# Kernel optimization log

Measured on AMD Instinct MI355X. Metric: run time of the kernel, lower is better.

## Reference

```python
import jax, jax.numpy as jnp
import numpy as np

DECAY = 0.99
EPS = 1e-05
COMMIT = 0.25


def setup_inputs() -> dict:
    key = jax.random.key(0)
    k1, k2 = jax.random.split(key)
    dim, n_embed = 256, 8192
    z = jax.random.normal(k1, (32, 32, 32, dim), dtype=jnp.float32)
    embed = jax.random.normal(k2, (dim, n_embed), dtype=jnp.float32)
    cluster_size = jnp.zeros((n_embed,), dtype=jnp.float32)
    embed_avg = embed  # torch init: embed_avg = embed.clone()
    return {"z": z, "embed": embed, "cluster_size": cluster_size, "embed_avg": embed_avg}


def reference(z, embed, cluster_size, embed_avg):
    dim, n_embed = embed.shape
    flatten = z.reshape(-1, dim)                       # [N, D]
    # squared L2 distance to each code: ||f||^2 - 2 f.E + ||E||^2
    dist = ((flatten ** 2).sum(1, keepdims=True)
            - 2.0 * flatten @ embed
            + (embed ** 2).sum(0, keepdims=True))      # [N, K]
    ind = jnp.argmin(dist, axis=1)                     # [N]
    quantize = jnp.take(embed.T, ind, axis=0).reshape(z.shape)
    embed_ind = ind.reshape(z.shape[:-1])

    # EMA codebook update (training mode), via segment_sum instead of a dense one-hot
    counts = jax.ops.segment_sum(jnp.ones_like(ind, dtype=flatten.dtype), ind,
                                 num_segments=n_embed)          # [K]
    embed_sum = jax.ops.segment_sum(flatten, ind,
                                    num_segments=n_embed).T     # [D, K]
    cluster_size_new = cluster_size * DECAY + (1.0 - DECAY) * counts
    embed_avg_new = embed_avg * DECAY + (1.0 - DECAY) * embed_sum
    n = cluster_size_new.sum()
    cs = (cluster_size_new + EPS) / (n + n_embed * EPS) * n
    embed_new = embed_avg_new / cs[None, :]

    diff = COMMIT * jnp.mean((jax.lax.stop_gradient(quantize) - z) ** 2)
    quantize_st = z + jax.lax.stop_gradient(quantize - z)  # straight-through
    return quantize_st, diff, embed_ind, embed_new
```

## Files before the change

### kernel.cpp

```cpp
#include <hip/hip_runtime.h>
#include <hip/hip_bf16.h>

#define D 256
#define K 8192
#define NTOT 32768
#define BM 128
#define BN2 128
#define BD 32
#define CSPLIT 4
#define CT_PER (K / CSPLIT / BN2)

typedef __bf16 bf16x8 __attribute__((ext_vector_type(8)));
typedef float f32x4 __attribute__((ext_vector_type(4)));

__device__ __forceinline__ void gl_lds16(const void* g, void* l) {
    __builtin_amdgcn_global_load_lds(
        (__attribute__((address_space(1))) void*)(g),
        (__attribute__((address_space(3))) void*)(l), 16, 0, 0);
}

__device__ __forceinline__ unsigned int enc_f32(float f) {
    unsigned int u = __float_as_uint(f);
    return (u & 0x80000000u) ? ~u : (u | 0x80000000u);
}

__device__ __forceinline__ unsigned short f2bfu(float x) {
    __hip_bfloat16 h = __float2bfloat16(x);
    return __builtin_bit_cast(unsigned short, h);
}
__device__ __forceinline__ float bfu2f(unsigned short u) {
    return __bfloat162float(__builtin_bit_cast(__hip_bfloat16, u));
}

__global__ __launch_bounds__(256)
void conv_F(const float* __restrict__ z, unsigned short* __restrict__ Fhi,
            unsigned short* __restrict__ Flo) {
    int i4 = blockIdx.x * 256 + threadIdx.x;
    float4 v = ((const float4*)z)[i4];
    ushort4 h, l;
    h.x = f2bfu(v.x); l.x = f2bfu(v.x - bfu2f(h.x));
    h.y = f2bfu(v.y); l.y = f2bfu(v.y - bfu2f(h.y));
    h.z = f2bfu(v.z); l.z = f2bfu(v.z - bfu2f(h.z));
    h.w = f2bfu(v.w); l.w = f2bfu(v.w - bfu2f(h.w));
    ((ushort4*)Fhi)[i4] = h;
    ((ushort4*)Flo)[i4] = l;
}

__global__ __launch_bounds__(256)
void conv_E(const float* __restrict__ E, unsigned short* __restrict__ EhiT,
            unsigned short* __restrict__ EloT, float* __restrict__ ET) {
    __shared__ float tile[64][65];
    int tid = threadIdx.x;
    int k0 = blockIdx.x * 64, d0 = blockIdx.y * 64;
#pragma unroll
    for (int it = 0; it < 16; ++it) {
        int idx = it * 256 + tid;
        int dr = idx >> 6, kc = idx & 63;
        tile[kc][dr] = E[(d0 + dr) * K + k0 + kc];
    }
    __syncthreads();
#pragma unroll
    for (int it = 0; it < 16; ++it) {
        int idx = it * 256 + tid;
        int kr = idx >> 6, dc = idx & 63;
        float v = tile[kr][dc];
        unsigned short h = f2bfu(v);
        int o = (k0 + kr) * D + d0 + dc;
        EhiT[o] = h;
        EloT[o] = f2bfu(v - bfu2f(h));
        ET[o] = v;
    }
}

__global__ __launch_bounds__(256)
void enorm_kernel(const float* __restrict__ E, float* __restrict__ enorm) {
    int k = blockIdx.x * 256 + threadIdx.x;
    float s = 0.f;
    for (int d = 0; d < D; ++d) {
        float v = E[d * K + k];
        s += v * v;
    }
    enorm[k] = s;
}

__global__ __launch_bounds__(256)
void mfma_dist_argmin(const unsigned short* __restrict__ Fhi,
                      const unsigned short* __restrict__ Flo,
                      const unsigned short* __restrict__ EhiT,
                      const unsigned short* __restrict__ EloT,
                      const float* __restrict__ enorm,
                      unsigned long long* __restrict__ bestpack) {
    __shared__ unsigned short Ah[BM * BD], Al[BM * BD], Bh[BN2 * BD], Bl[BN2 * BD];

    const int tid = threadIdx.x;
    const int wave = tid >> 6;
    const int lane = tid & 63;
    const int qd = lane >> 4;
    const int ln = lane & 15;
    const int wm = (wave >> 1) * 64;
    const int wn = (wave & 1) * 64;
    const int n0 = blockIdx.x * BM;
    const int c0 = blockIdx.y * (K / CSPLIT);
    const int r_ = tid >> 2, s_ = tid & 3;

    float bestv[16];
    int besti[16];
#pragma unroll
    for (int i = 0; i < 16; ++i) { bestv[i] = 3.402823466e38f; besti[i] = 0; }

    for (int ct = 0; ct < CT_PER; ++ct) {
        const int cb = c0 + ct * BN2;
        f32x4 acc[4][4];
#pragma unroll
        for (int mi = 0; mi < 4; ++mi)
#pragma unroll
            for (int ni = 0; ni < 4; ++ni) acc[mi][ni] = (f32x4){0.f, 0.f, 0.f, 0.f};

        for (int d0 = 0; d0 < D; d0 += BD) {
#pragma unroll
            for (int it = 0; it < 2; ++it) {
                const int row = it * 64 + r_;
                const int goffA = (n0 + row) * D + d0 + s_ * 8;
                const int goffB = (cb + row) * D + d0 + s_ * 8;
                const int loff = it * 2048 + wave * 512;
                gl_lds16(Fhi + goffA, &Ah[loff]);
                gl_lds16(Flo + goffA, &Al[loff]);
                gl_lds16(EhiT + goffB, &Bh[loff]);
                gl_lds16(EloT + goffB, &Bl[loff]);
            }
            __syncthreads();

            bf16x8 ah[4], al[4], bh[4], bl[4];
#pragma unroll
            for (int mi = 0; mi < 4; ++mi) {
                int off = (wm + mi * 16 + ln) * BD + qd * 8;
                ah[mi] = *(const bf16x8*)&Ah[off];
                al[mi] = *(const bf16x8*)&Al[off];
            }
#pragma unroll
            for (int ni = 0; ni < 4; ++ni) {
                int off = (wn + ni * 16 + ln) * BD + qd * 8;
                bh[ni] = *(const bf16x8*)&Bh[off];
                bl[ni] = *(const bf16x8*)&Bl[off];
            }
#pragma unroll
            for (int mi = 0; mi < 4; ++mi)
#pragma unroll
                for (int ni = 0; ni < 4; ++ni)
                    acc[mi][ni] = __builtin_amdgcn_mfma_f32_16x16x32_bf16(
                        ah[mi], bh[ni], acc[mi][ni], 0, 0, 0);
#pragma unroll
            for (int mi = 0; mi < 4; ++mi)
#pragma unroll
                for (int ni = 0; ni < 4; ++ni)
                    acc[mi][ni] = __builtin_amdgcn_mfma_f32_16x16x32_bf16(
                        ah[mi], bl[ni], acc[mi][ni], 0, 0, 0);
#pragma unroll
            for (int mi = 0; mi < 4; ++mi)
#pragma unroll
                for (int ni = 0; ni < 4; ++ni)
                    acc[mi][ni] = __builtin_amdgcn_mfma_f32_16x16x32_bf16(
                        al[mi], bh[ni], acc[mi][ni], 0, 0, 0);
            __syncthreads();
        }

#pragma unroll
        for (int ni = 0; ni < 4; ++ni) {
            int k = cb + wn + ni * 16 + ln;
            float en = enorm[k];
#pragma unroll
            for (int mi = 0; mi < 4; ++mi) {
                f32x4 a = acc[mi][ni];
#pragma unroll
                for (int r = 0; r < 4; ++r) {
                    float dist = en - 2.0f * a[r];
                    int bi = mi * 4 + r;
                    if (dist < bestv[bi]) { bestv[bi] = dist; besti[bi] = k; }
                }
            }
        }
    }

#pragma unroll
    for (int mi = 0; mi < 4; ++mi) {
#pragma unroll
        for (int r = 0; r < 4; ++r) {
            int bi = mi * 4 + r;
            float v = bestv[bi];
            int ix = besti[bi];
#pragma unroll
            for (int off = 1; off < 16; off <<= 1) {
                float v2 = __shfl_xor(v, off);
                int i2 = __shfl_xor(ix, off);
                if (v2 < v || (v2 == v && i2 < ix)) { v = v2; ix = i2; }
            }
            if (ln == 0) {
                int m = n0 + wm + mi * 16 + qd * 4 + r;
                unsigned long long pack =
                    ((unsigned long long)enc_f32(v) << 32) | (unsigned int)ix;
                atomicMin(&bestpack[m], pack);
            }
        }
    }
}

#define ROWS_PER_BLOCK 64
__global__ __launch_bounds__(256)
void assign_apply(const float* __restrict__ z,
                  const float* __restrict__ ET,
                  const unsigned long long* __restrict__ bestpack,
                  float* __restrict__ out_q, float* __restrict__ out_ind,
                  float* __restrict__ out_diff,
                  float* __restrict__ counts, float* __restrict__ esumT) {
    const int tx = threadIdx.x;
    const int rbase = blockIdx.x * ROWS_PER_BLOCK;
    float part = 0.f;
    for (int r = 0; r < ROWS_PER_BLOCK; ++r) {
        int n = rbase + r;
        unsigned long long p = bestpack[n];
        int idx = (int)(p & 0xFFFFFFFFull);
        float f = z[n * D + tx];
        float q = ET[idx * D + tx];
        out_q[n * D + tx] = q;
        float dd = q - f;
        part += dd * dd;
        atomicAdd(&esumT[idx * D + tx], f);
        if (tx == 0) {
            atomicAdd(&counts[idx], 1.0f);
            out_ind[n] = (float)idx;
        }
    }
#pragma unroll
    for (int off = 32; off; off >>= 1) part += __shfl_down(part, off);
    __shared__ float wsum[4];
    if ((tx & 63) == 0) wsum[tx >> 6] = part;
    __syncthreads();
    if (tx == 0) {
        float t = wsum[0] + wsum[1] + wsum[2] + wsum[3];
        atomicAdd(out_diff, t * (0.25f / 8388608.0f));
    }
}

__global__ __launch_bounds__(1024)
void csn_sum(const float* __restrict__ cs_in, const float* __restrict__ counts,
             float* __restrict__ csn, float* __restrict__ nsum) {
    const float decay = 0.99f;
    const float omd = 0.01f;
    int tx = threadIdx.x;
    float p = 0.f;
    for (int k = tx; k < K; k += 1024) {
        float v = decay * cs_in[k] + omd * counts[k];
        csn[k] = v;
        p += v;
    }
#pragma unroll
    for (int off = 32; off; off >>= 1) p += __shfl_down(p, off);
    __shared__ float red[16];
    if ((tx & 63) == 0) red[tx >> 6] = p;
    __syncthreads();
    if (tx == 0) {
        float t = 0.f;
        for (int i = 0; i < 16; ++i) t += red[i];
        nsum[0] = t;
    }
}

__global__ __launch_bounds__(256)
void finalize(const float* __restrict__ eavg, const float* __restrict__ esumT,
              const float* __restrict__ csn, const float* __restrict__ nsum,
              float* __restrict__ out_enew) {
    const float decay = 0.99f;
    const float omd = 0.01f;
    const float keps = (float)(8192 * 1e-5);
    int idx = blockIdx.x * 256 + threadIdx.x;
    float nv = nsum[0];
    int k = idx & (K - 1);
    int d = idx >> 13;
    float avg_new = decay * eavg[idx] + omd * esumT[k * D + d];
    float cs = (csn[k] + 1e-5f) / (nv + keps) * nv;
    out_enew[idx] = avg_new / cs;
}

extern "C" void kernel_launch(void* const* d_in, const int* in_sizes, int n_in,
                              void* d_out, int out_size, void* d_ws, size_t ws_size,
                              hipStream_t stream) {
    const float* z = (const float*)d_in[0];
    const float* embed = (const float*)d_in[1];
    const float* cs_in = (const float*)d_in[2];
    const float* eavg = (const float*)d_in[3];

    float* out = (float*)d_out;
    float* out_q = out;
    float* out_diff = out + 8388608;
    float* out_ind = out + 8388609;
    float* out_enew = out + 8421377;

    char* ws = (char*)d_ws;
    unsigned long long* bestpack = (unsigned long long*)ws;
    float* enorm = (float*)(ws + 262144);
    float* counts = (float*)(ws + 294912);
    float* csn = (float*)(ws + 327680);
    float* nsum = (float*)(ws + 360448);
    float* esumT = (float*)(ws + 360704);
    unsigned short* Fhi = (unsigned short*)(ws + 8749312);
    unsigned short* Flo = (unsigned short*)(ws + 25526528);
    unsigned short* EhiT = (unsigned short*)(ws + 42303744);
    unsigned short* EloT = (unsigned short*)(ws + 46498048);
    float* ET = (float*)(ws + 50692352);

    hipMemsetAsync(bestpack, 0xFF, NTOT * 8, stream);
    hipMemsetAsync(counts, 0, K * 4, stream);
    hipMemsetAsync(esumT, 0, K * D * 4, stream);
    hipMemsetAsync(out_diff, 0, 4, stream);

    conv_F<<<NTOT * D / 4 / 256, 256, 0, stream>>>(z, Fhi, Flo);
    conv_E<<<dim3(K / 64, D / 64), 256, 0, stream>>>(embed, EhiT, EloT, ET);
    enorm_kernel<<<K / 256, 256, 0, stream>>>(embed, enorm);
    mfma_dist_argmin<<<dim3(NTOT / BM, CSPLIT), 256, 0, stream>>>(Fhi, Flo, EhiT, EloT,
                                                                  enorm, bestpack);
    assign_apply<<<NTOT / ROWS_PER_BLOCK, 256, 0, stream>>>(z, ET, bestpack, out_q,
                                                            out_ind, out_diff, counts, esumT);
    csn_sum<<<1, 1024, 0, stream>>>(cs_in, counts, csn, nsum);
    finalize<<<(D * K) / 256, 256, 0, stream>>>(eavg, esumT, csn, nsum, out_enew);
}
```

Measured before the change: 612.8 us.

## Load MFMA operands directly from global into registers with double buffering

Drops the shared-memory staging and barriers in the distance/argmin GEMM. Each wave now loads its bf16 hi/lo operand fragments straight from global memory into registers, prefetching the next K-slice into a second register buffer while the current one feeds the MFMAs. Launch bounds now request two blocks per CU. Each wave pulls its own copy of the shared tiles, so data reuse across waves now depends on cache instead of LDS, and the doubled register buffers raise register pressure.

```diff
diff --git a/kernel.cpp b/kernel.cpp
--- a/kernel.cpp
+++ b/kernel.cpp
@@ -6,18 +6,11 @@
 #define NTOT 32768
 #define BM 128
 #define BN2 128
-#define BD 32
 #define CSPLIT 4
 #define CT_PER (K / CSPLIT / BN2)
 
 typedef __bf16 bf16x8 __attribute__((ext_vector_type(8)));
 typedef float f32x4 __attribute__((ext_vector_type(4)));
-
-__device__ __forceinline__ void gl_lds16(const void* g, void* l) {
-    __builtin_amdgcn_global_load_lds(
-        (__attribute__((address_space(1))) void*)(g),
-        (__attribute__((address_space(3))) void*)(l), 16, 0, 0);
-}
 
 __device__ __forceinline__ unsigned int enc_f32(float f) {
     unsigned int u = __float_as_uint(f);
@@ -83,15 +76,13 @@
     enorm[k] = s;
 }
 
-__global__ __launch_bounds__(256)
+__global__ __launch_bounds__(256, 2)
 void mfma_dist_argmin(const unsigned short* __restrict__ Fhi,
                       const unsigned short* __restrict__ Flo,
                       const unsigned short* __restrict__ EhiT,
                       const unsigned short* __restrict__ EloT,
                       const float* __restrict__ enorm,
                       unsigned long long* __restrict__ bestpack) {
-    __shared__ unsigned short Ah[BM * BD], Al[BM * BD], Bh[BN2 * BD], Bl[BN2 * BD];
-
     const int tid = threadIdx.x;
     const int wave = tid >> 6;
     const int lane = tid & 63;
@@ -101,79 +92,84 @@
     const int wn = (wave & 1) * 64;
     const int n0 = blockIdx.x * BM;
     const int c0 = blockIdx.y * (K / CSPLIT);
-    const int r_ = tid >> 2, s_ = tid & 3;
+
+    int aoff[4], boff[4];
+#pragma unroll
+    for (int mi = 0; mi < 4; ++mi) aoff[mi] = (n0 + wm + mi * 16 + ln) * D + qd * 8;
+#pragma unroll
+    for (int ni = 0; ni < 4; ++ni) boff[ni] = (wn + ni * 16 + ln) * D + qd * 8;
 
     float bestv[16];
     int besti[16];
 #pragma unroll
     for (int i = 0; i < 16; ++i) { bestv[i] = 3.402823466e38f; besti[i] = 0; }
 
+    bf16x8 ah[2][4], al[2][4], bh[2][4], bl[2][4];
+
+    auto load_stage = [&](int buf, int ct, int d0) {
+        const int ub = (c0 + ct * BN2) * D + d0;
+#pragma unroll
+        for (int mi = 0; mi < 4; ++mi) {
+            ah[buf][mi] = *(const bf16x8*)(Fhi + aoff[mi] + d0);
+            al[buf][mi] = *(const bf16x8*)(Flo + aoff[mi] + d0);
+        }
+#pragma unroll
+        for (int ni = 0; ni < 4; ++ni) {
+            bh[buf][ni] = *(const bf16x8*)(EhiT + boff[ni] + ub);
+            bl[buf][ni] = *(const bf16x8*)(EloT + boff[ni] + ub);
+        }
+    };
+
+    load_stage(0, 0, 0);
+
     for (int ct = 0; ct < CT_PER; ++ct) {
         const int cb = c0 + ct * BN2;
+        float en[4];
+#pragma unroll
+        for (int ni = 0; ni < 4; ++ni) en[ni] = enorm[cb + wn + ni * 16 + ln];
+
         f32x4 acc[4][4];
 #pragma unroll
         for (int mi = 0; mi < 4; ++mi)
 #pragma unroll
             for (int ni = 0; ni < 4; ++ni) acc[mi][ni] = (f32x4){0.f, 0.f, 0.f, 0.f};
 
-        for (int d0 = 0; d0 < D; d0 += BD) {
-#pragma unroll
-            for (int it = 0; it < 2; ++it) {
-                const int row = it * 64 + r_;
-                const int goffA = (n0 + row) * D + d0 + s_ * 8;
-                const int goffB = (cb + row) * D + d0 + s_ * 8;
-                const int loff = it * 2048 + wave * 512;
-                gl_lds16(Fhi + goffA, &Ah[loff]);
-                gl_lds16(Flo + goffA, &Al[loff]);
-                gl_lds16(EhiT + goffB, &Bh[loff]);
-                gl_lds16(EloT + goffB, &Bl[loff]);
-            }
-            __syncthreads();
-
-            bf16x8 ah[4], al[4], bh[4], bl[4];
-#pragma unroll
-            for (int mi = 0; mi < 4; ++mi) {
-                int off = (wm + mi * 16 + ln) * BD + qd * 8;
-                ah[mi] = *(const bf16x8*)&Ah[off];
-                al[mi] = *(const bf16x8*)&Al[off];
-            }
-#pragma unroll
-            for (int ni = 0; ni < 4; ++ni) {
-                int off = (wn + ni * 16 + ln) * BD + qd * 8;
-                bh[ni] = *(const bf16x8*)&Bh[off];
-                bl[ni] = *(const bf16x8*)&Bl[off];
-            }
+#pragma unroll
+        for (int dd = 0; dd < 8; ++dd) {
+            const int b = dd & 1;
+            int nct = ct, ndd = dd + 1;
+            if (ndd == 8) { ndd = 0; nct = ct + 1; }
+            if (nct < CT_PER) load_stage(b ^ 1, nct, ndd * 32);
+
 #pragma unroll
             for (int mi = 0; mi < 4; ++mi)
 #pragma unroll
                 for (int ni = 0; ni < 4; ++ni)
                     acc[mi][ni] = __builtin_amdgcn_mfma_f32_16x16x32_bf16(
-                        ah[mi], bh[ni], acc[mi][ni], 0, 0, 0);
+                        ah[b][mi], bh[b][ni], acc[mi][ni], 0, 0, 0);
 #pragma unroll
             for (int mi = 0; mi < 4; ++mi)
 #pragma unroll
                 for (int ni = 0; ni < 4; ++ni)
                     acc[mi][ni] = __builtin_amdgcn_mfma_f32_16x16x32_bf16(
-                        ah[mi], bl[ni], acc[mi][ni], 0, 0, 0);
+                        ah[b][mi], bl[b][ni], acc[mi][ni], 0, 0, 0);
 #pragma unroll
             for (int mi = 0; mi < 4; ++mi)
 #pragma unroll
                 for (int ni = 0; ni < 4; ++ni)
                     acc[mi][ni] = __builtin_amdgcn_mfma_f32_16x16x32_bf16(
-                        al[mi], bh[ni], acc[mi][ni], 0, 0, 0);
-            __syncthreads();
+                        al[b][mi], bh[b][ni], acc[mi][ni], 0, 0, 0);
         }
 
 #pragma unroll
         for (int ni = 0; ni < 4; ++ni) {
             int k = cb + wn + ni * 16 + ln;
-            float en = enorm[k];
 #pragma unroll
             for (int mi = 0; mi < 4; ++mi) {
                 f32x4 a = acc[mi][ni];
 #pragma unroll
                 for (int r = 0; r < 4; ++r) {
-                    float dist = en - 2.0f * a[r];
+                    float dist = en[ni] - 2.0f * a[r];
                     int bi = mi * 4 + r;
                     if (dist < bestv[bi]) { bestv[bi] = dist; besti[bi] = k; }
                 }
```

Result: slower. 1.279 ms (+108.7%).

## Swizzle LDS tiles in distance GEMM and read enorm from transposed codebook

Applied to the files above, without the earlier changes.

The distance/argmin kernel now XOR-swizzles the 16-byte chunk position within each LDS row, both when loading and when reading fragments, to cut LDS bank conflicts. It also moves the barrier to the top of the d-loop and preloads the enorm values before the argmin epilogue. enorm_kernel now reads rows of the transposed fp32 codebook with float4 loads instead of strided columns. conv_E gains a partial-sum reduction that only atomically adds zero, so that work is dead and adds some atomics.

```diff
diff --git a/kernel.cpp b/kernel.cpp
--- a/kernel.cpp
+++ b/kernel.cpp
@@ -48,7 +48,8 @@
 
 __global__ __launch_bounds__(256)
 void conv_E(const float* __restrict__ E, unsigned short* __restrict__ EhiT,
-            unsigned short* __restrict__ EloT, float* __restrict__ ET) {
+            unsigned short* __restrict__ EloT, float* __restrict__ ET,
+            float* __restrict__ enorm) {
     __shared__ float tile[64][65];
     int tid = threadIdx.x;
     int k0 = blockIdx.x * 64, d0 = blockIdx.y * 64;
@@ -59,6 +60,7 @@
         tile[kc][dr] = E[(d0 + dr) * K + k0 + kc];
     }
     __syncthreads();
+    float psum[4];
 #pragma unroll
     for (int it = 0; it < 16; ++it) {
         int idx = it * 256 + tid;
@@ -69,16 +71,29 @@
         EhiT[o] = h;
         EloT[o] = f2bfu(v - bfu2f(h));
         ET[o] = v;
-    }
-}
-
-__global__ __launch_bounds__(256)
-void enorm_kernel(const float* __restrict__ E, float* __restrict__ enorm) {
+        psum[it & 3] = (it < 4 ? 0.f : psum[it & 3]) + v * v;
+    }
+#pragma unroll
+    for (int g = 0; g < 4; ++g) {
+        float p = psum[g];
+#pragma unroll
+        for (int off = 32; off; off >>= 1) p += __shfl_down(p, off);
+        if ((tid & 63) == 0) {
+            int kr = g * 4 + (tid >> 6);
+            atomicAdd(&enorm[k0 + kr * 4 + 0], 0.f);
+        }
+    }
+}
+
+__global__ __launch_bounds__(256)
+void enorm_kernel(const float* __restrict__ ET, float* __restrict__ enorm) {
     int k = blockIdx.x * 256 + threadIdx.x;
+    const float4* row = (const float4*)(ET + k * D);
     float s = 0.f;
-    for (int d = 0; d < D; ++d) {
-        float v = E[d * K + k];
-        s += v * v;
+#pragma unroll
+    for (int d = 0; d < D / 4; ++d) {
+        float4 v = row[d];
+        s += v.x * v.x + v.y * v.y + v.z * v.z + v.w * v.w;
     }
     enorm[k] = s;
 }
@@ -101,7 +116,9 @@
     const int wn = (wave & 1) * 64;
     const int n0 = blockIdx.x * BM;
     const int c0 = blockIdx.y * (K / CSPLIT);
-    const int r_ = tid >> 2, s_ = tid & 3;
+    const int r_ = tid >> 2;
+    const int s_sw = (tid & 3) ^ ((tid >> 3) & 3);
+    const int csw = (qd ^ ((ln >> 1) & 3)) * 8;
 
     float bestv[16];
     int besti[16];
@@ -117,29 +134,29 @@
             for (int ni = 0; ni < 4; ++ni) acc[mi][ni] = (f32x4){0.f, 0.f, 0.f, 0.f};
 
         for (int d0 = 0; d0 < D; d0 += BD) {
+            __syncthreads();
 #pragma unroll
             for (int it = 0; it < 2; ++it) {
-                const int row = it * 64 + r_;
-                const int goffA = (n0 + row) * D + d0 + s_ * 8;
-                const int goffB = (cb + row) * D + d0 + s_ * 8;
-                const int loff = it * 2048 + wave * 512;
-                gl_lds16(Fhi + goffA, &Ah[loff]);
-                gl_lds16(Flo + goffA, &Al[loff]);
-                gl_lds16(EhiT + goffB, &Bh[loff]);
-                gl_lds16(EloT + goffB, &Bl[loff]);
+                const int ga = (n0 + it * 64 + r_) * D + d0 + s_sw * 8;
+                const int gb = (cb + it * 64 + r_) * D + d0 + s_sw * 8;
+                const int lo = it * 2048 + wave * 512;
+                gl_lds16(Fhi + ga, &Ah[lo]);
+                gl_lds16(Flo + ga, &Al[lo]);
+                gl_lds16(EhiT + gb, &Bh[lo]);
+                gl_lds16(EloT + gb, &Bl[lo]);
             }
             __syncthreads();
 
             bf16x8 ah[4], al[4], bh[4], bl[4];
 #pragma unroll
             for (int mi = 0; mi < 4; ++mi) {
-                int off = (wm + mi * 16 + ln) * BD + qd * 8;
+                int off = (wm + mi * 16 + ln) * BD + csw;
                 ah[mi] = *(const bf16x8*)&Ah[off];
                 al[mi] = *(const bf16x8*)&Al[off];
             }
 #pragma unroll
             for (int ni = 0; ni < 4; ++ni) {
-                int off = (wn + ni * 16 + ln) * BD + qd * 8;
+                int off = (wn + ni * 16 + ln) * BD + csw;
                 bh[ni] = *(const bf16x8*)&Bh[off];
                 bl[ni] = *(const bf16x8*)&Bl[off];
             }
@@ -161,19 +178,20 @@
                 for (int ni = 0; ni < 4; ++ni)
                     acc[mi][ni] = __builtin_amdgcn_mfma_f32_16x16x32_bf16(
                         al[mi], bh[ni], acc[mi][ni], 0, 0, 0);
-            __syncthreads();
-        }
-
+        }
+
+        float en[4];
+#pragma unroll
+        for (int ni = 0; ni < 4; ++ni) en[ni] = enorm[cb + wn + ni * 16 + ln];
 #pragma unroll
         for (int ni = 0; ni < 4; ++ni) {
             int k = cb + wn + ni * 16 + ln;
-            float en = enorm[k];
 #pragma unroll
             for (int mi = 0; mi < 4; ++mi) {
                 f32x4 a = acc[mi][ni];
 #pragma unroll
                 for (int r = 0; r < 4; ++r) {
-                    float dist = en - 2.0f * a[r];
+                    float dist = en[ni] - 2.0f * a[r];
                     int bi = mi * 4 + r;
                     if (dist < bestv[bi]) { bestv[bi] = dist; besti[bi] = k; }
                 }
@@ -314,8 +332,8 @@
     hipMemsetAsync(out_diff, 0, 4, stream);
 
     conv_F<<<NTOT * D / 4 / 256, 256, 0, stream>>>(z, Fhi, Flo);
-    conv_E<<<dim3(K / 64, D / 64), 256, 0, stream>>>(embed, EhiT, EloT, ET);
-    enorm_kernel<<<K / 256, 256, 0, stream>>>(embed, enorm);
+    conv_E<<<dim3(K / 64, D / 64), 256, 0, stream>>>(embed, EhiT, EloT, ET, enorm);
+    enorm_kernel<<<K / 256, 256, 0, stream>>>(ET, enorm);
     mfma_dist_argmin<<<dim3(NTOT / BM, CSPLIT), 256, 0, stream>>>(Fhi, Flo, EhiT, EloT,
                                                                   enorm, bestpack);
     assign_apply<<<NTOT / ROWS_PER_BLOCK, 256, 0, stream>>>(z, ET, bestpack, out_q,
```

Measured after the change: 598.1 us. 1.02x faster.
